# Optimization experiments

Hardware: AMD Instinct MI355X
Metric: run time of the kernel (lower is better)

The kernel has to match this reference:

```python
import jax, jax.numpy as jnp
import numpy as np

# dims
N = 50000      # total nodes in merged batch graph
M = 250000     # edges for GNN propagation
E = 200000     # candidate edges scored by mixture-Bernoulli head
MAXN = 512     # max_num_nodes (padded adjacency row length)
H = 128        # hidden_dim = embedding_dim = msg_dim
EF = 128       # edge_feat_dim = 2 * att_edge_dim
ATT = 128      # att_hidden_dim
K = 20         # num_mix_component
L = 3          # num_GNN_layers
S = 512        # num_subgraph
B = 16         # batch of graphs
C = 1          # num_canonical_order


def setup_inputs() -> dict:
    key = jax.random.key(0)
    ks = list(jax.random.split(key, 64))
    it = iter(ks)
    nk = lambda: next(it)
    d = {}
    d['node_feat'] = jax.random.normal(nk(), (N, MAXN), jnp.float32)
    d['edge'] = jax.random.randint(nk(), (M, 2), 0, N, dtype=jnp.int32)
    d['edge_feat'] = jax.random.normal(nk(), (M, EF), jnp.float32)
    d['node_idx_gnn'] = jax.random.randint(nk(), (E, 2), 0, N, dtype=jnp.int32)
    d['label'] = (jax.random.uniform(nk(), (E,)) < 0.1).astype(jnp.float32)
    # even sorted partition of E candidate edges into S subgraphs (all nonempty)
    d['subgraph_idx'] = ((jnp.arange(E) * S) // E).astype(jnp.int32)
    # bc_idx = repeat_interleave(arange(B*C), subgraphs_per_graph)
    d['bc_idx'] = jnp.repeat(jnp.arange(B * C, dtype=jnp.int32), S // (B * C))
    # params
    def lin(k, out_d, in_d):
        return jax.random.normal(k, (out_d, in_d), jnp.float32) * (1.0 / np.sqrt(in_d))
    d['dec_W'] = lin(nk(), H, MAXN); d['dec_b'] = jnp.zeros((H,), jnp.float32)
    d['msg_W1'] = jnp.stack([lin(nk(), H, H + EF) for _ in range(L)])
    d['msg_b1'] = jnp.zeros((L, H), jnp.float32)
    d['msg_W2'] = jnp.stack([lin(nk(), H, H) for _ in range(L)])
    d['msg_b2'] = jnp.zeros((L, H), jnp.float32)
    d['att_W1'] = jnp.stack([lin(nk(), ATT, H + EF) for _ in range(L)])
    d['att_b1'] = jnp.zeros((L, ATT), jnp.float32)
    d['att_W2'] = jnp.stack([lin(nk(), H, ATT) for _ in range(L)])
    d['att_b2'] = jnp.zeros((L, H), jnp.float32)
    d['gru_Wih'] = jnp.stack([lin(nk(), 3 * H, H) for _ in range(L)])
    d['gru_bih'] = jnp.zeros((L, 3 * H), jnp.float32)
    d['gru_Whh'] = jnp.stack([lin(nk(), 3 * H, H) for _ in range(L)])
    d['gru_bhh'] = jnp.zeros((L, 3 * H), jnp.float32)
    d['th_W1'] = lin(nk(), H, H); d['th_b1'] = jnp.zeros((H,), jnp.float32)
    d['th_W2'] = lin(nk(), H, H); d['th_b2'] = jnp.zeros((H,), jnp.float32)
    d['th_W3'] = lin(nk(), K, H); d['th_b3'] = jnp.zeros((K,), jnp.float32)
    d['al_W1'] = lin(nk(), H, H); d['al_b1'] = jnp.zeros((H,), jnp.float32)
    d['al_W2'] = lin(nk(), H, H); d['al_b2'] = jnp.zeros((H,), jnp.float32)
    d['al_W3'] = lin(nk(), K, H); d['al_b3'] = jnp.zeros((K,), jnp.float32)
    return d


def _gran_forward(node_feat, edge_feat, label, dec_W, dec_b, msg_W1, msg_b1,
                  msg_W2, msg_b2, att_W1, att_b1, att_W2, att_b2, gru_Wih,
                  gru_bih, gru_Whh, gru_bhh, th_W1, th_b1, th_W2, th_b2,
                  th_W3, th_b3, al_W1, al_b1, al_W2, al_b2, al_W3, al_b3,
                  edge, node_idx_gnn, subgraph_idx, bc_idx):
    n = node_feat.shape[0]
    # decoder_input: Linear(max_num_nodes -> embedding_dim)
    state = node_feat @ dec_W.T + dec_b  # [N, H]
    src, dst = edge[:, 0], edge[:, 1]
    for l in range(L):
        if l > 0:
            state = jax.nn.relu(state)
        # _prop: gather diff, msg MLP, sigmoid attention gate, scatter-sum, GRU
        diff = state[src] - state[dst]                       # [M, H]
        ei = jnp.concatenate([diff, edge_feat], axis=1)      # [M, H+EF]
        msg = jax.nn.relu(ei @ msg_W1[l].T + msg_b1[l]) @ msg_W2[l].T + msg_b2[l]
        att = jax.nn.sigmoid(jax.nn.relu(ei @ att_W1[l].T + att_b1[l]) @ att_W2[l].T + att_b2[l])
        agg = jax.ops.segment_sum(msg * att, dst, num_segments=n)  # [N, H]
        # torch GRUCell
        gi = agg @ gru_Wih[l].T + gru_bih[l]
        gh = state @ gru_Whh[l].T + gru_bhh[l]
        i_r, i_z, i_n = jnp.split(gi, 3, axis=-1)
        h_r, h_z, h_n = jnp.split(gh, 3, axis=-1)
        r = jax.nn.sigmoid(i_r + h_r)
        z = jax.nn.sigmoid(i_z + h_z)
        nn_ = jnp.tanh(i_n + r * h_n)
        state = (1.0 - z) * nn_ + z * state
    # mixture-Bernoulli heads on candidate-edge node-state diffs
    d2 = state[node_idx_gnn[:, 0]] - state[node_idx_gnn[:, 1]]  # [E, H]
    def mlp3(x, W1, b1, W2, b2, W3, b3):
        h = jax.nn.relu(x @ W1.T + b1)
        h = jax.nn.relu(h @ W2.T + b2)
        return h @ W3.T + b3
    log_theta = mlp3(d2, th_W1, th_b1, th_W2, th_b2, th_W3, th_b3)  # [E, K]
    log_alpha = mlp3(d2, al_W1, al_b1, al_W2, al_b2, al_W3, al_b3)  # [E, K]
    # mixture_bernoulli_loss (pos_weight = 1.0)
    y = label[:, None]
    adj_loss = jax.nn.softplus(-log_theta) + (1.0 - y) * log_theta  # BCEWithLogits, [E, K]
    const = jax.ops.segment_sum(jnp.ones((label.shape[0],), log_theta.dtype), subgraph_idx, num_segments=S)
    reduce_adj = jax.ops.segment_sum(adj_loss, subgraph_idx, num_segments=S)     # [S, K]
    reduce_la = jax.ops.segment_sum(log_alpha, subgraph_idx, num_segments=S)
    reduce_la = jax.nn.log_softmax(reduce_la / const[:, None], axis=-1)
    log_prob = jax.scipy.special.logsumexp(-reduce_adj + reduce_la, axis=1)      # [S]
    bc_log_prob = jax.ops.segment_sum(log_prob, bc_idx, num_segments=B * C)
    bc_const = jax.ops.segment_sum(const, bc_idx, num_segments=B * C)
    bc_loss = (bc_log_prob / bc_const).reshape(B, C)
    b_loss = jax.scipy.special.logsumexp(bc_loss, axis=1)  # logsumexp over orderings
    return jnp.mean(-b_loss)


def reference(node_feat, edge, edge_feat, node_idx_gnn, label, subgraph_idx,
              bc_idx, dec_W, dec_b, msg_W1, msg_b1, msg_W2, msg_b2, att_W1,
              att_b1, att_W2, att_b2, gru_Wih, gru_bih, gru_Whh, gru_bhh,
              th_W1, th_b1, th_W2, th_b2, th_W3, th_b3, al_W1, al_b1, al_W2,
              al_b2, al_W3, al_b3):
    return _gran_forward(node_feat, edge_feat, label, dec_W, dec_b, msg_W1,
                         msg_b1, msg_W2, msg_b2, att_W1, att_b1, att_W2,
                         att_b2, gru_Wih, gru_bih, gru_Whh, gru_bhh, th_W1,
                         th_b1, th_W2, th_b2, th_W3, th_b3, al_W1, al_b1,
                         al_W2, al_b2, al_W3, al_b3, edge, node_idx_gnn,
                         subgraph_idx, bc_idx)
```

## Files before the change

### kernel.cpp

```cpp
#include <hip/hip_runtime.h>
#include <cstdint>
#include <cstddef>


typedef __bf16 bf16x8 __attribute__((ext_vector_type(8)));
typedef short  s16x8  __attribute__((ext_vector_type(8)));
typedef short  s16x4  __attribute__((ext_vector_type(4)));
typedef float  f32x4  __attribute__((ext_vector_type(4)));

__device__ inline unsigned short f2bf(float f) {
    return __builtin_bit_cast(unsigned short, (__bf16)f);
}
__device__ inline float bf2f(unsigned short b) {
    return __uint_as_float(((unsigned int)b) << 16);
}
__device__ inline unsigned int pk2(float a, float b) {
    return ((unsigned int)f2bf(b) << 16) | f2bf(a);
}
__device__ inline f32x4 MFMA(bf16x8 a, bf16x8 b, f32x4 c) {
    return __builtin_amdgcn_mfma_f32_16x16x32_bf16(a, b, c, 0, 0, 0);
}

__device__ inline bf16x8 ld_swz(const char* lds, int row, int unit) {
    return *(const bf16x8*)(lds + row * 256 + ((unit ^ (row & 7)) << 4));
}
__device__ inline void hid_write(char* HID, int h0, int erow, s16x4 s4) {
    int unit = h0 >> 3;
    *(s16x4*)(HID + erow * 256 + ((unit ^ (erow & 7)) << 4) + ((h0 & 4) << 1)) = s4;
}
__device__ inline bf16x8 ldA(const short* __restrict__ Wb, int K, int row, int koff) {
    return *(const bf16x8*)(Wb + (size_t)row * K + koff);
}
__device__ inline bf16x8 ld_f32_frag(const float* __restrict__ p) {
    float4 a = *(const float4*)p, b = *(const float4*)(p + 4);
    s16x8 s;
    s[0] = f2bf(a.x); s[1] = f2bf(a.y); s[2] = f2bf(a.z); s[3] = f2bf(a.w);
    s[4] = f2bf(b.x); s[5] = f2bf(b.y); s[6] = f2bf(b.z); s[7] = f2bf(b.w);
    return __builtin_bit_cast(bf16x8, s);
}

#define NPACK 31
struct PrepackArgs {
    const float* src[NPACK];
    short*       dst[NPACK];
    int stride[NPACK];
    int rows[NPACK];
    int rowsTot[NPACK];
    int cols[NPACK];
};

__global__ void prepack(PrepackArgs a) {
    int e = blockIdx.y;
    int row = blockIdx.x;
    if (row >= a.rowsTot[e]) return;
    int c8 = threadIdx.x;
    if (c8 * 8 >= a.cols[e]) return;
    s16x8 s = {};
    if (row < a.rows[e]) {
        const float* p = a.src[e] + (size_t)row * a.stride[e] + c8 * 8;
        float4 x = *(const float4*)p, y = *(const float4*)(p + 4);
        s[0] = f2bf(x.x); s[1] = f2bf(x.y); s[2] = f2bf(x.z); s[3] = f2bf(x.w);
        s[4] = f2bf(y.x); s[5] = f2bf(y.y); s[6] = f2bf(y.z); s[7] = f2bf(y.w);
    }
    *(s16x8*)(a.dst[e] + (size_t)row * a.cols[e] + c8 * 8) = s;
}

__device__ inline void proj_gemm_store(const char* ST, char* PJ,
                                       const short* __restrict__ projW,
                                       short* __restrict__ proj,
                                       int rb, int R, int tid)
{
    const int l = tid & 63, w = tid >> 6;
    f32x4 accP[2][2][4] = {};
#pragma unroll
    for (int ks = 0; ks < 4; ++ks) {
        int koff = ks * 32 + (l >> 4) * 8;
        bf16x8 aw[2][2];
#pragma unroll
        for (int pc = 0; pc < 2; ++pc)
#pragma unroll
            for (int mt = 0; mt < 2; ++mt)
                aw[pc][mt] = ldA(projW, 128, pc * 128 + 32 * w + 16 * mt + (l & 15), koff);
#pragma unroll
        for (int n = 0; n < 4; ++n) {
            bf16x8 b = ld_swz(ST, 16 * n + (l & 15), ks * 4 + (l >> 4));
#pragma unroll
            for (int pc = 0; pc < 2; ++pc)
#pragma unroll
                for (int mt = 0; mt < 2; ++mt)
                    accP[pc][mt][n] = MFMA(aw[pc][mt], b, accP[pc][mt][n]);
        }
    }
    const int half = w >> 1;
#pragma unroll
    for (int hh = 0; hh < 2; ++hh) {
        __syncthreads();
        if (half == hh) {
#pragma unroll
            for (int pc = 0; pc < 2; ++pc)
#pragma unroll
                for (int mt = 0; mt < 2; ++mt) {
                    int h0 = 32 * w + 16 * mt + ((l >> 4) << 2);
                    int colp = 2 * h0 + 4 * pc - 128 * hh;
#pragma unroll
                    for (int n = 0; n < 4; ++n) {
                        f32x4 v = accP[pc][mt][n];
                        s16x4 s4;
                        s4[0] = f2bf(v[0]); s4[1] = f2bf(v[1]);
                        s4[2] = f2bf(v[2]); s4[3] = f2bf(v[3]);
                        hid_write(PJ, colp, 16 * n + (l & 15), s4);
                    }
                }
        }
        __syncthreads();
#pragma unroll
        for (int p2 = 0; p2 < 4; ++p2) {
            int row = p2 * 16 + (tid >> 4);
            int r = rb + row;
            if (r < R) {
                bf16x8 v = ld_swz(PJ, row, tid & 15);
                *(s16x8*)(proj + (size_t)r * 256 + hh * 128 + (tid & 15) * 8) =
                    __builtin_bit_cast(s16x8, v);
            }
        }
    }
}

__global__ __launch_bounds__(256, 2)
void dec_proj(const float* __restrict__ nf, int R,
              const short* __restrict__ decWb, const float* __restrict__ bias,
              const short* __restrict__ projW,
              short* __restrict__ sOut, short* __restrict__ proj)
{
    __shared__ char ST[16384];
    __shared__ char PJ[16384];
    const int tid = threadIdx.x, l = tid & 63, w = tid >> 6;
    const int rb = blockIdx.x * 64;

    const float* brow[4];
#pragma unroll
    for (int n = 0; n < 4; ++n) {
        int row = rb + 16 * n + (l & 15); if (row >= R) row = R - 1;
        brow[n] = nf + (size_t)row * 512;
    }

    f32x4 acc[2][4] = {};
    for (int kc = 0; kc < 512; kc += 128) {
#pragma unroll
        for (int ks = 0; ks < 4; ++ks) {
            int koff = kc + ks * 32 + (l >> 4) * 8;
            bf16x8 a0 = ldA(decWb, 512, 32 * w + (l & 15), koff);
            bf16x8 a1 = ldA(decWb, 512, 32 * w + 16 + (l & 15), koff);
#pragma unroll
            for (int n = 0; n < 4; ++n) {
                bf16x8 b = ld_f32_frag(brow[n] + koff);
                acc[0][n] = MFMA(a0, b, acc[0][n]);
                acc[1][n] = MFMA(a1, b, acc[1][n]);
            }
        }
    }
#pragma unroll
    for (int mt = 0; mt < 2; ++mt) {
        int c0 = 32 * w + 16 * mt + ((l >> 4) << 2);
        float4 bv = *(const float4*)&bias[c0];
#pragma unroll
        for (int n = 0; n < 4; ++n) {
            f32x4 v = acc[mt][n];
            s16x4 s4;
            s4[0] = f2bf(v[0] + bv.x); s4[1] = f2bf(v[1] + bv.y);
            s4[2] = f2bf(v[2] + bv.z); s4[3] = f2bf(v[3] + bv.w);
            hid_write(ST, c0, 16 * n + (l & 15), s4);
        }
    }
    __syncthreads();
#pragma unroll
    for (int p2 = 0; p2 < 4; ++p2) {
        int row = p2 * 16 + (tid >> 4);
        int r = rb + row;
        if (r < R) {
            bf16x8 v = ld_swz(ST, row, tid & 15);
            *(s16x8*)(sOut + (size_t)r * 128 + (tid & 15) * 8) =
                __builtin_bit_cast(s16x8, v);
        }
    }
    proj_gemm_store(ST, PJ, projW, proj, rb, R, tid);
}

template<int HAS_PROJ>
__global__ __launch_bounds__(256, 2)
void node_fused(const short* __restrict__ aggb, const short* __restrict__ sin_,
                const short* __restrict__ Wih, const short* __restrict__ Whh,
                const float* __restrict__ bih, const float* __restrict__ bhh,
                const short* __restrict__ projW,
                short* __restrict__ sOut, short* __restrict__ proj, int R)
{
    __shared__ char ST[16384];
    __shared__ char PJ[16384];
    const int tid = threadIdx.x, l = tid & 63, w = tid >> 6;
    const int rb = blockIdx.x * 64;

    const short* arow[4];
    const short* srow[4];
#pragma unroll
    for (int n = 0; n < 4; ++n) {
        int row = rb + 16 * n + (l & 15); if (row >= R) row = R - 1;
        arow[n] = aggb + (size_t)row * 128;
        srow[n] = sin_ + (size_t)row * 128;
    }
    s16x4 svv[2][4];
#pragma unroll
    for (int mt = 0; mt < 2; ++mt) {
        int c0 = 32 * w + 16 * mt + ((l >> 4) << 2);
#pragma unroll
        for (int n = 0; n < 4; ++n)
            svv[mt][n] = *(const s16x4*)(srow[n] + c0);
    }

    unsigned int rpk[2][4][2], zpk[2][4][2];

    for (int p = 0; p < 3; ++p) {
        f32x4 gia[2][4] = {}, gha[2][4] = {};
#pragma unroll
        for (int ks = 0; ks < 4; ++ks) {
            int koff = ks * 32 + (l >> 4) * 8;
            bf16x8 ai0 = ldA(Wih, 128, p * 128 + 32 * w + (l & 15), koff);
            bf16x8 ai1 = ldA(Wih, 128, p * 128 + 32 * w + 16 + (l & 15), koff);
            bf16x8 ah0 = ldA(Whh, 128, p * 128 + 32 * w + (l & 15), koff);
            bf16x8 ah1 = ldA(Whh, 128, p * 128 + 32 * w + 16 + (l & 15), koff);
#pragma unroll
            for (int n = 0; n < 4; ++n) {
                bf16x8 ba = *(const bf16x8*)(arow[n] + koff);
                bf16x8 bs = *(const bf16x8*)(srow[n] + koff);
                gia[0][n] = MFMA(ai0, ba, gia[0][n]);
                gia[1][n] = MFMA(ai1, ba, gia[1][n]);
                gha[0][n] = MFMA(ah0, bs, gha[0][n]);
                gha[1][n] = MFMA(ah1, bs, gha[1][n]);
            }
        }
#pragma unroll
        for (int mt = 0; mt < 2; ++mt) {
            int c0 = 32 * w + 16 * mt + ((l >> 4) << 2);
            float4 bi = *(const float4*)&bih[p * 128 + c0];
            float4 bh = *(const float4*)&bhh[p * 128 + c0];
            float biv[4] = {bi.x, bi.y, bi.z, bi.w};
            float bhv[4] = {bh.x, bh.y, bh.z, bh.w};
#pragma unroll
            for (int n = 0; n < 4; ++n) {
                float gv[4], hv[4];
#pragma unroll
                for (int q = 0; q < 4; ++q) {
                    gv[q] = gia[mt][n][q] + biv[q];
                    hv[q] = gha[mt][n][q] + bhv[q];
                }
                if (p == 0) {
                    rpk[mt][n][0] = pk2(1.f / (1.f + expf(-(gv[0] + hv[0]))),
                                        1.f / (1.f + expf(-(gv[1] + hv[1]))));
                    rpk[mt][n][1] = pk2(1.f / (1.f + expf(-(gv[2] + hv[2]))),
                                        1.f / (1.f + expf(-(gv[3] + hv[3]))));
                } else if (p == 1) {
                    zpk[mt][n][0] = pk2(1.f / (1.f + expf(-(gv[0] + hv[0]))),
                                        1.f / (1.f + expf(-(gv[1] + hv[1]))));
                    zpk[mt][n][1] = pk2(1.f / (1.f + expf(-(gv[2] + hv[2]))),
                                        1.f / (1.f + expf(-(gv[3] + hv[3]))));
                } else {
                    s16x4 s4;
#pragma unroll
                    for (int q = 0; q < 4; ++q) {
                        unsigned int ru = rpk[mt][n][q >> 1], zu = zpk[mt][n][q >> 1];
                        float r = bf2f((unsigned short)((q & 1) ? (ru >> 16) : (ru & 0xffffu)));
                        float z = bf2f((unsigned short)((q & 1) ? (zu >> 16) : (zu & 0xffffu)));
                        float nn = tanhf(gv[q] + r * hv[q]);
                        float o = (1.f - z) * nn + z * bf2f((unsigned short)svv[mt][n][q]);
                        s4[q] = f2bf(HAS_PROJ ? fmaxf(o, 0.f) : o);
                    }
                    hid_write(ST, c0, 16 * n + (l & 15), s4);
                }
            }
        }
    }
    __syncthreads();
#pragma unroll
    for (int p2 = 0; p2 < 4; ++p2) {
        int row = p2 * 16 + (tid >> 4);
        int r = rb + row;
        if (r < R) {
            bf16x8 v = ld_swz(ST, row, tid & 15);
            *(s16x8*)(sOut + (size_t)r * 128 + (tid & 15) * 8) =
                __builtin_bit_cast(s16x8, v);
        }
    }
    if (HAS_PROJ)
        proj_gemm_store(ST, PJ, projW, proj, rb, R, tid);
}

__global__ __launch_bounds__(256, 3)
void edge_fused2(const short* __restrict__ efc,
                 const int* __restrict__ srcs, const int* __restrict__ dsts,
                 const short* __restrict__ proj,
                 const short* __restrict__ mW1b, const short* __restrict__ mW2,
                 const short* __restrict__ aW1b, const short* __restrict__ aW2,
                 const float* __restrict__ mb1, const float* __restrict__ mb2,
                 const float* __restrict__ ab1, const float* __restrict__ ab2,
                 short* __restrict__ msgatt, int M, int ntiles)
{
    __shared__ char HIDm[16384];
    __shared__ char HIDa[16384];
    const int tid = threadIdx.x, l = tid & 63, w = tid >> 6;
    int q = ntiles >> 3, r = ntiles & 7;
    int xcd = blockIdx.x & 7, o = blockIdx.x >> 3;
    int tile = (xcd < r ? xcd * (q + 1) : r * (q + 1) + (xcd - r) * q) + o;
    const int pb = tile * 64;

    const char* erow[4];
    s16x8 psv[2][4], pdv[2][4];
    {
#pragma unroll
        for (int n = 0; n < 4; ++n) {
            int pos = pb + 16 * n + (l & 15); if (pos >= M) pos = M - 1;
            int sv = srcs[pos], dv = dsts[pos];
            erow[n] = (const char*)(efc + (size_t)pos * 128);
#pragma unroll
            for (int mt = 0; mt < 2; ++mt) {
                int off = 2 * (32 * w + 16 * mt + ((l >> 4) << 2));
                psv[mt][n] = *(const s16x8*)(proj + (size_t)sv * 256 + off);
                pdv[mt][n] = *(const s16x8*)(proj + (size_t)dv * 256 + off);
            }
        }
    }

    f32x4 accm[2][4] = {}, acca[2][4] = {};
#pragma unroll
    for (int ks = 0; ks < 4; ++ks) {
        int koff = ks * 32 + (l >> 4) * 8;
        bf16x8 am0 = ldA(mW1b, 128, 32 * w + (l & 15), koff);
        bf16x8 am1 = ldA(mW1b, 128, 32 * w + 16 + (l & 15), koff);
        bf16x8 aa0 = ldA(aW1b, 128, 32 * w + (l & 15), koff);
        bf16x8 aa1 = ldA(aW1b, 128, 32 * w + 16 + (l & 15), koff);
#pragma unroll
        for (int n = 0; n < 4; ++n) {
            bf16x8 b = *(const bf16x8*)(erow[n] + koff * 2);
            accm[0][n] = MFMA(am0, b, accm[0][n]);
            accm[1][n] = MFMA(am1, b, accm[1][n]);
            acca[0][n] = MFMA(aa0, b, acca[0][n]);
            acca[1][n] = MFMA(aa1, b, acca[1][n]);
        }
    }
#pragma unroll
    for (int mt = 0; mt < 2; ++mt) {
        int h0 = 32 * w + 16 * mt + ((l >> 4) << 2);
        float4 bm = *(const float4*)&mb1[h0];
        float4 ba = *(const float4*)&ab1[h0];
        float bmv[4] = {bm.x, bm.y, bm.z, bm.w};
        float bav[4] = {ba.x, ba.y, ba.z, ba.w};
#pragma unroll
        for (int n = 0; n < 4; ++n) {
            s16x8 ps = psv[mt][n], pd = pdv[mt][n];
            f32x4 vm = accm[mt][n], va = acca[mt][n];
            s16x4 sm, sa;
#pragma unroll
            for (int qq = 0; qq < 4; ++qq) {
                float m_ = vm[qq] + bmv[qq] + bf2f((unsigned short)ps[qq])
                           - bf2f((unsigned short)pd[qq]);
                float a_ = va[qq] + bav[qq] + bf2f((unsigned short)ps[qq + 4])
                           - bf2f((unsigned short)pd[qq + 4]);
                sm[qq] = f2bf(fmaxf(m_, 0.f));
                sa[qq] = f2bf(fmaxf(a_, 0.f));
            }
            hid_write(HIDm, h0, 16 * n + (l & 15), sm);
            hid_write(HIDa, h0, 16 * n + (l & 15), sa);
        }
    }
    __syncthreads();

    f32x4 acc2m[2][4] = {}, acc2a[2][4] = {};
#pragma unroll
    for (int ks = 0; ks < 4; ++ks) {
        int koff = ks * 32 + (l >> 4) * 8;
        bf16x8 wm0 = ldA(mW2, 128, 32 * w + (l & 15), koff);
        bf16x8 wm1 = ldA(mW2, 128, 32 * w + 16 + (l & 15), koff);
        bf16x8 wa0 = ldA(aW2, 128, 32 * w + (l & 15), koff);
        bf16x8 wa1 = ldA(aW2, 128, 32 * w + 16 + (l & 15), koff);
#pragma unroll
        for (int n = 0; n < 4; ++n) {
            bf16x8 bm = ld_swz(HIDm, 16 * n + (l & 15), ks * 4 + (l >> 4));
            bf16x8 ba = ld_swz(HIDa, 16 * n + (l & 15), ks * 4 + (l >> 4));
            acc2m[0][n] = MFMA(wm0, bm, acc2m[0][n]);
            acc2m[1][n] = MFMA(wm1, bm, acc2m[1][n]);
            acc2a[0][n] = MFMA(wa0, ba, acc2a[0][n]);
            acc2a[1][n] = MFMA(wa1, ba, acc2a[1][n]);
        }
    }
    __syncthreads();
#pragma unroll
    for (int mt = 0; mt < 2; ++mt) {
        int c0 = 32 * w + 16 * mt + ((l >> 4) << 2);
        float4 bm2 = *(const float4*)&mb2[c0];
        float4 ba2 = *(const float4*)&ab2[c0];
#pragma unroll
        for (int n = 0; n < 4; ++n) {
            f32x4 m_ = acc2m[mt][n], a_ = acc2a[mt][n];
            float o0 = (m_[0] + bm2.x) / (1.f + expf(-(a_[0] + ba2.x)));
            float o1 = (m_[1] + bm2.y) / (1.f + expf(-(a_[1] + ba2.y)));
            float o2 = (m_[2] + bm2.z) / (1.f + expf(-(a_[2] + ba2.z)));
            float o3 = (m_[3] + bm2.w) / (1.f + expf(-(a_[3] + ba2.w)));
            s16x4 s4;
            s4[0] = f2bf(o0); s4[1] = f2bf(o1); s4[2] = f2bf(o2); s4[3] = f2bf(o3);
            hid_write(HIDm, c0, 16 * n + (l & 15), s4);
        }
    }
    __syncthreads();
#pragma unroll
    for (int p2 = 0; p2 < 4; ++p2) {
        int row = p2 * 16 + (tid >> 4);
        int pos = pb + row;
        if (pos < M) {
            bf16x8 v = ld_swz(HIDm, row, tid & 15);
            *(s16x8*)(msgatt + (size_t)pos * 128 + (tid & 15) * 8) =
                __builtin_bit_cast(s16x8, v);
        }
    }
}

__global__ __launch_bounds__(256, 4)
void mlp_loss(const short* __restrict__ sP, const int* __restrict__ gidx,
              const float* __restrict__ label, const int* __restrict__ sg,
              const short* __restrict__ thW1, const short* __restrict__ thW2,
              const short* __restrict__ thW3,
              const float* __restrict__ thb1, const float* __restrict__ thb2,
              const float* __restrict__ thb3,
              const short* __restrict__ alW1, const short* __restrict__ alW2,
              const short* __restrict__ alW3,
              const float* __restrict__ alb1, const float* __restrict__ alb2,
              const float* __restrict__ alb3,
              float* __restrict__ radj, float* __restrict__ rla,
              float* __restrict__ cntS, int E, int S)
{
    __shared__ char D2T[16384];
    __shared__ char HID[16384];
    __shared__ float sadj[2][20];
    __shared__ float sla[2][20];
    __shared__ float scnt[2];
    __shared__ int sbase;
    const int tid = threadIdx.x, l = tid & 63, w = tid >> 6;
    const int eb = blockIdx.x * 64;

    if (tid == 0) sbase = sg[eb];
    if (tid < 40) { sadj[tid / 20][tid % 20] = 0.f; sla[tid / 20][tid % 20] = 0.f; }
    if (tid < 2) scnt[tid] = 0.f;

    for (int i = tid; i < 64 * 16; i += 256) {
        int row = i >> 4, u = i & 15;
        int e = eb + row; if (e >= E) e = E - 1;
        int2 ab = *(const int2*)&gidx[2 * (size_t)e];
        s16x8 x = *(const s16x8*)(sP + (size_t)ab.x * 128 + u * 8);
        s16x8 y = *(const s16x8*)(sP + (size_t)ab.y * 128 + u * 8);
        s16x8 d;
#pragma unroll
        for (int j = 0; j < 8; ++j)
            d[j] = f2bf(bf2f((unsigned short)x[j]) - bf2f((unsigned short)y[j]));
        *(s16x8*)(D2T + row * 256 + ((u ^ (row & 7)) << 4)) = d;
    }
    __syncthreads();

    for (int pass = 0; pass < 2; ++pass) {
        const short* W1 = pass ? alW1 : thW1;
        const short* W2 = pass ? alW2 : thW2;
        const short* W3 = pass ? alW3 : thW3;
        const float* b1 = pass ? alb1 : thb1;
        const float* b2 = pass ? alb2 : thb2;
        const float* b3 = pass ? alb3 : thb3;

        f32x4 acc[2][4] = {};
#pragma unroll
        for (int ks = 0; ks < 4; ++ks) {
            int koff = ks * 32 + (l >> 4) * 8;
            bf16x8 a0 = ldA(W1, 128, 32 * w + (l & 15), koff);
            bf16x8 a1 = ldA(W1, 128, 32 * w + 16 + (l & 15), koff);
#pragma unroll
            for (int n = 0; n < 4; ++n) {
                bf16x8 b = ld_swz(D2T, 16 * n + (l & 15), ks * 4 + (l >> 4));
                acc[0][n] = MFMA(a0, b, acc[0][n]);
                acc[1][n] = MFMA(a1, b, acc[1][n]);
            }
        }
        __syncthreads();
#pragma unroll
        for (int mt = 0; mt < 2; ++mt) {
            int h0 = 32 * w + 16 * mt + ((l >> 4) << 2);
            float4 bv = *(const float4*)&b1[h0];
#pragma unroll
            for (int n = 0; n < 4; ++n) {
                f32x4 v = acc[mt][n];
                s16x4 s4;
                s4[0] = f2bf(fmaxf(v[0] + bv.x, 0.f));
                s4[1] = f2bf(fmaxf(v[1] + bv.y, 0.f));
                s4[2] = f2bf(fmaxf(v[2] + bv.z, 0.f));
                s4[3] = f2bf(fmaxf(v[3] + bv.w, 0.f));
                hid_write(HID, h0, 16 * n + (l & 15), s4);
            }
        }
        __syncthreads();
        f32x4 acc2[2][4] = {};
#pragma unroll
        for (int ks = 0; ks < 4; ++ks) {
            int koff = ks * 32 + (l >> 4) * 8;
            bf16x8 a0 = ldA(W2, 128, 32 * w + (l & 15), koff);
            bf16x8 a1 = ldA(W2, 128, 32 * w + 16 + (l & 15), koff);
#pragma unroll
            for (int n = 0; n < 4; ++n) {
                bf16x8 b = ld_swz(HID, 16 * n + (l & 15), ks * 4 + (l >> 4));
                acc2[0][n] = MFMA(a0, b, acc2[0][n]);
                acc2[1][n] = MFMA(a1, b, acc2[1][n]);
            }
        }
        __syncthreads();
#pragma unroll
        for (int mt = 0; mt < 2; ++mt) {
            int h0 = 32 * w + 16 * mt + ((l >> 4) << 2);
            float4 bv = *(const float4*)&b2[h0];
#pragma unroll
            for (int n = 0; n < 4; ++n) {
                f32x4 v = acc2[mt][n];
                s16x4 s4;
                s4[0] = f2bf(fmaxf(v[0] + bv.x, 0.f));
                s4[1] = f2bf(fmaxf(v[1] + bv.y, 0.f));
                s4[2] = f2bf(fmaxf(v[2] + bv.z, 0.f));
                s4[3] = f2bf(fmaxf(v[3] + bv.w, 0.f));
                hid_write(HID, h0, 16 * n + (l & 15), s4);
            }
        }
        __syncthreads();
        f32x4 acc3[2] = {};
#pragma unroll
        for (int ks = 0; ks < 4; ++ks) {
            int koff = ks * 32 + (l >> 4) * 8;
            bf16x8 a0 = ldA(W3, 128, (l & 15), koff);
            bf16x8 a1 = ldA(W3, 128, 16 + (l & 15), koff);
            bf16x8 b = ld_swz(HID, 16 * w + (l & 15), ks * 4 + (l >> 4));
            acc3[0] = MFMA(a0, b, acc3[0]);
            acc3[1] = MFMA(a1, b, acc3[1]);
        }
        {
            int e = eb + 16 * w + (l & 15);
            if (e < E) {
                int ls = sg[e] - sbase;
                if (ls < 0) ls = 0; if (ls > 1) ls = 1;
                float y = (pass == 0) ? label[e] : 0.f;
#pragma unroll
                for (int mt = 0; mt < 2; ++mt) {
                    int c0 = 16 * mt + ((l >> 4) << 2);
                    if (c0 < 20) {
#pragma unroll
                        for (int qq = 0; qq < 4; ++qq) {
                            int k = c0 + qq;
                            if (k < 20) {
                                float t = acc3[mt][qq] + b3[k];
                                if (pass == 0) {
                                    float sp = fmaxf(-t, 0.f) + log1pf(expf(-fabsf(t)));
                                    atomicAdd(&sadj[ls][k], sp + (1.f - y) * t);
                                } else {
                                    atomicAdd(&sla[ls][k], t);
                                }
                            }
                        }
                    }
                }
            }
        }
        __syncthreads();
    }

    if (tid < 64) {
        int e = eb + tid;
        if (e < E) {
            int ls = sg[e] - sbase;
            if (ls >= 0 && ls < 2) atomicAdd(&scnt[ls], 1.f);
        }
    }
    __syncthreads();
    if (tid < 40) {
        int ls = tid / 20, k = tid % 20;
        int s = sbase + ls;
        if (s < S) {
            float v = sadj[ls][k], v2 = sla[ls][k];
            if (v  != 0.f) atomicAdd(&radj[s * 20 + k], v);
            if (v2 != 0.f) atomicAdd(&rla[s * 20 + k], v2);
        }
    }
    if (tid < 2) {
        int s = sbase + tid;
        if (s < S && scnt[tid] != 0.f) atomicAdd(&cntS[s], scnt[tid]);
    }
}

__global__ void csr_count(const int* __restrict__ edge, int* __restrict__ cnt, int M) {
    int e = blockIdx.x * 256 + threadIdx.x;
    if (e < M) atomicAdd(&cnt[edge[2 * (size_t)e + 1]], 1);
}

__global__ void csr_scan(const int* __restrict__ cnt, int* __restrict__ rowptr,
                         int* __restrict__ wofs, int N)
{
    __shared__ int part[1024];
    int t = threadIdx.x;
    int chunk = (N + 1023) / 1024;
    int b0 = t * chunk, b1 = b0 + chunk; if (b1 > N) b1 = N; if (b0 > N) b0 = N;
    int s = 0;
    for (int i = b0; i < b1; ++i) s += cnt[i];
    part[t] = s;
    __syncthreads();
    for (int off = 1; off < 1024; off <<= 1) {
        int v = (t >= off) ? part[t - off] : 0;
        __syncthreads();
        part[t] += v;
        __syncthreads();
    }
    int run = (t ? part[t - 1] : 0);
    for (int i = b0; i < b1; ++i) { rowptr[i] = run; wofs[i] = run; run += cnt[i]; }
    if (t == 1023) rowptr[N] = run;
}

__global__ void csr_scatter2(const int* __restrict__ edge, int* __restrict__ wofs,
                             int* __restrict__ eidx, int* __restrict__ srcs,
                             int* __restrict__ dsts, int M)
{
    int e = blockIdx.x * 256 + threadIdx.x;
    if (e < M) {
        int2 sd = *(const int2*)&edge[2 * (size_t)e];
        int p = atomicAdd(&wofs[sd.y], 1);
        eidx[p] = e; srcs[p] = sd.x; dsts[p] = sd.y;
    }
}

__global__ void ef_gather(const float* __restrict__ ef, const int* __restrict__ eidx,
                          short* __restrict__ efc, int M)
{
    long i = (long)blockIdx.x * 256 + threadIdx.x;
    if (i >= (long)M * 16) return;
    int p = (int)(i >> 4), u = (int)(i & 15);
    int e = eidx[p];
    const float* sp = ef + (size_t)e * 128 + u * 8;
    float4 a = *(const float4*)sp, b = *(const float4*)(sp + 4);
    s16x8 s;
    s[0] = f2bf(a.x); s[1] = f2bf(a.y); s[2] = f2bf(a.z); s[3] = f2bf(a.w);
    s[4] = f2bf(b.x); s[5] = f2bf(b.y); s[6] = f2bf(b.z); s[7] = f2bf(b.w);
    *(s16x8*)(efc + (size_t)p * 128 + u * 8) = s;
}

__global__ __launch_bounds__(256)
void agg_gather3(const short* __restrict__ msgatt, const int* __restrict__ rowptr,
                 short* __restrict__ aggb, int N)
{
    int wid = blockIdx.x * 4 + (threadIdx.x >> 6);
    int l = threadIdx.x & 63;
    int v = wid * 4 + (l >> 4);
    int u = l & 15;
    if (v >= N) return;
    int b = rowptr[v], e = rowptr[v + 1];
    float acc[8] = {};
    for (int i = b; i < e; ++i) {
        s16x8 x = *(const s16x8*)(msgatt + (size_t)i * 128 + u * 8);
#pragma unroll
        for (int j = 0; j < 8; ++j) acc[j] += bf2f((unsigned short)x[j]);
    }
    s16x8 o;
#pragma unroll
    for (int j = 0; j < 8; ++j) o[j] = f2bf(acc[j]);
    *(s16x8*)(aggb + (size_t)v * 128 + u * 8) = o;
}

__global__ void final_kernel(const float* __restrict__ radj, const float* __restrict__ rla,
                             const float* __restrict__ cnt, const int* __restrict__ bc_idx,
                             float* __restrict__ out)
{
    __shared__ float bcl[16], bcc[16];
    const int s = threadIdx.x;
    if (s < 16) { bcl[s] = 0.f; bcc[s] = 0.f; }
    __syncthreads();
    float c = cnt[s];
    float x[20];
    float mx = -1e30f;
#pragma unroll
    for (int k = 0; k < 20; ++k) { x[k] = rla[s * 20 + k] / c; mx = fmaxf(mx, x[k]); }
    float se = 0.f;
#pragma unroll
    for (int k = 0; k < 20; ++k) se += expf(x[k] - mx);
    float lse = mx + logf(se);
    float t[20];
    float m2 = -1e30f;
#pragma unroll
    for (int k = 0; k < 20; ++k) { t[k] = -radj[s * 20 + k] + x[k] - lse; m2 = fmaxf(m2, t[k]); }
    float s2 = 0.f;
#pragma unroll
    for (int k = 0; k < 20; ++k) s2 += expf(t[k] - m2);
    float lp = m2 + logf(s2);
    atomicAdd(&bcl[bc_idx[s]], lp);
    atomicAdd(&bcc[bc_idx[s]], c);
    __syncthreads();
    if (s == 0) {
        float a = 0.f;
        for (int b = 0; b < 16; ++b) a += bcl[b] / bcc[b];
        out[0] = -a / 16.f;
    }
}

extern "C" void kernel_launch(void* const* d_in, const int* in_sizes, int n_in,
                              void* d_out, int out_size, void* d_ws, size_t ws_size,
                              hipStream_t stream)
{
    const float* node_feat = (const float*)d_in[0];
    const int*   edge      = (const int*)  d_in[1];
    const float* edge_feat = (const float*)d_in[2];
    const int*   gnn_idx   = (const int*)  d_in[3];
    const float* label     = (const float*)d_in[4];
    const int*   sg_idx    = (const int*)  d_in[5];
    const int*   bc_idx    = (const int*)  d_in[6];
    const float* dec_W  = (const float*)d_in[7];
    const float* dec_b  = (const float*)d_in[8];
    const float* msg_W1 = (const float*)d_in[9];
    const float* msg_b1 = (const float*)d_in[10];
    const float* msg_W2 = (const float*)d_in[11];
    const float* msg_b2 = (const float*)d_in[12];
    const float* att_W1 = (const float*)d_in[13];
    const float* att_b1 = (const float*)d_in[14];
    const float* att_W2 = (const float*)d_in[15];
    const float* att_b2 = (const float*)d_in[16];
    const float* gru_Wih = (const float*)d_in[17];
    const float* gru_bih = (const float*)d_in[18];
    const float* gru_Whh = (const float*)d_in[19];
    const float* gru_bhh = (const float*)d_in[20];
    const float* th_W1 = (const float*)d_in[21];
    const float* th_b1 = (const float*)d_in[22];
    const float* th_W2 = (const float*)d_in[23];
    const float* th_b2 = (const float*)d_in[24];
    const float* th_W3 = (const float*)d_in[25];
    const float* th_b3 = (const float*)d_in[26];
    const float* al_W1 = (const float*)d_in[27];
    const float* al_b1 = (const float*)d_in[28];
    const float* al_W2 = (const float*)d_in[29];
    const float* al_b2 = (const float*)d_in[30];
    const float* al_W3 = (const float*)d_in[31];
    const float* al_b3 = (const float*)d_in[32];

    const int N = in_sizes[0] / 512;
    const int M = in_sizes[1] / 2;
    const int E = in_sizes[3] / 2;
    const int S = in_sizes[6];

    size_t off = 0;
    auto alloc = [&](size_t bytes) {
        char* p = (char*)d_ws + off;
        off += (bytes + 255) & ~(size_t)255;
        return p;
    };
    short* decWb  = (short*)alloc((size_t)128 * 512 * 2);
    short* projWb = (short*)alloc((size_t)3 * 256 * 128 * 2);
    short* mW1bB  = (short*)alloc((size_t)3 * 128 * 128 * 2);
    short* aW1bB  = (short*)alloc((size_t)3 * 128 * 128 * 2);
    short* mW2B   = (short*)alloc((size_t)3 * 128 * 128 * 2);
    short* aW2B   = (short*)alloc((size_t)3 * 128 * 128 * 2);
    short* gihB   = (short*)alloc((size_t)3 * 384 * 128 * 2);
    short* ghhB   = (short*)alloc((size_t)3 * 384 * 128 * 2);
    short* thW1B  = (short*)alloc((size_t)128 * 128 * 2);
    short* thW2B  = (short*)alloc((size_t)128 * 128 * 2);
    short* thW3B  = (short*)alloc((size_t)32 * 128 * 2);
    short* alW1B  = (short*)alloc((size_t)128 * 128 * 2);
    short* alW2B  = (short*)alloc((size_t)128 * 128 * 2);
    short* alW3B  = (short*)alloc((size_t)32 * 128 * 2);
    short* sA     = (short*)alloc((size_t)N * 128 * 2);
    short* sB     = (short*)alloc((size_t)N * 128 * 2);
    short* sP     = (short*)alloc((size_t)N * 128 * 2);
    short* efc    = (short*)alloc((size_t)M * 128 * 2);
    short* msgatt = (short*)alloc((size_t)M * 128 * 2);
    short* proj   = (short*)alloc((size_t)N * 256 * 2);
    short* aggb   = (short*)alloc((size_t)N * 128 * 2);
    int*   cntN   = (int*)  alloc((size_t)N * 4);
    int*   wofs   = (int*)  alloc((size_t)N * 4);
    int*   rowptr = (int*)  alloc((size_t)(N + 1) * 4);
    int*   eidx   = (int*)  alloc((size_t)M * 4);
    int*   srcs   = (int*)  alloc((size_t)M * 4);
    int*   dsts   = (int*)  alloc((size_t)M * 4);
    float* radj   = (float*)alloc((size_t)S * 20 * 4);
    float* rla    = (float*)alloc((size_t)S * 20 * 4);
    float* cntS   = (float*)alloc((size_t)S * 4);

    PrepackArgs pa;
    int ei = 0;
    auto add = [&](const float* s, short* d, int stride, int rows, int rowsTot, int cols) {
        pa.src[ei] = s; pa.dst[ei] = d; pa.stride[ei] = stride;
        pa.rows[ei] = rows; pa.rowsTot[ei] = rowsTot; pa.cols[ei] = cols; ++ei;
    };
    add(dec_W, decWb, 512, 128, 128, 512);
    for (int l = 0; l < 3; ++l) {
        add(msg_W1 + (size_t)l * 128 * 256,       projWb + (size_t)l * 256 * 128,          256, 128, 128, 128);
        add(att_W1 + (size_t)l * 128 * 256,       projWb + (size_t)l * 256 * 128 + 16384,  256, 128, 128, 128);
        add(msg_W1 + (size_t)l * 128 * 256 + 128, mW1bB + (size_t)l * 16384,               256, 128, 128, 128);
        add(att_W1 + (size_t)l * 128 * 256 + 128, aW1bB + (size_t)l * 16384,               256, 128, 128, 128);
        add(msg_W2 + (size_t)l * 16384,           mW2B + (size_t)l * 16384,                128, 128, 128, 128);
        add(att_W2 + (size_t)l * 16384,           aW2B + (size_t)l * 16384,                128, 128, 128, 128);
        add(gru_Wih + (size_t)l * 49152,          gihB + (size_t)l * 49152,                128, 384, 384, 128);
        add(gru_Whh + (size_t)l * 49152,          ghhB + (size_t)l * 49152,                128, 384, 384, 128);
    }
    add(th_W1, thW1B, 128, 128, 128, 128);
    add(th_W2, thW2B, 128, 128, 128, 128);
    add(th_W3, thW3B, 128, 20, 32, 128);
    add(al_W1, alW1B, 128, 128, 128, 128);
    add(al_W2, alW2B, 128, 128, 128, 128);
    add(al_W3, alW3B, 128, 20, 32, 128);

    const dim3 blk(256);
    const int gN64 = (N + 63) / 64;
    const int gE64 = (E + 63) / 64;
    const int gMt  = (M + 255) / 256;
    const int ntilesM = (M + 63) / 64;
    const int gAgg = (N + 15) / 16;

    hipMemsetAsync(radj, 0, (size_t)(S * 20 * 2 + S) * 4, stream);
    hipMemsetAsync(cntN, 0, (size_t)N * 4, stream);

    prepack<<<dim3(384, NPACK), dim3(64), 0, stream>>>(pa);

    csr_count   <<<gMt, blk, 0, stream>>>(edge, cntN, M);
    csr_scan    <<<1, 1024, 0, stream>>>(cntN, rowptr, wofs, N);
    csr_scatter2<<<gMt, blk, 0, stream>>>(edge, wofs, eidx, srcs, dsts, M);
    ef_gather   <<<(int)(((long)M * 16 + 255) / 256), blk, 0, stream>>>(edge_feat, eidx, efc, M);

    dec_proj<<<gN64, blk, 0, stream>>>(node_feat, N, decWb, dec_b, projWb, sA, proj);

    short* bufs[2] = { sA, sB };
    for (int l = 0; l < 3; ++l) {
        short* sin  = bufs[l & 1];
        short* sout = (l == 2) ? sP : bufs[(l + 1) & 1];
        edge_fused2<<<ntilesM, blk, 0, stream>>>(efc, srcs, dsts, proj,
            mW1bB + (size_t)l * 16384, mW2B + (size_t)l * 16384,
            aW1bB + (size_t)l * 16384, aW2B + (size_t)l * 16384,
            msg_b1 + l * 128, msg_b2 + l * 128,
            att_b1 + l * 128, att_b2 + l * 128,
            msgatt, M, ntilesM);
        agg_gather3<<<gAgg, blk, 0, stream>>>(msgatt, rowptr, aggb, N);
        if (l < 2) {
            node_fused<1><<<gN64, blk, 0, stream>>>(aggb, sin,
                gihB + (size_t)l * 49152, ghhB + (size_t)l * 49152,
                gru_bih + l * 384, gru_bhh + l * 384,
                projWb + (size_t)(l + 1) * 256 * 128, sout, proj, N);
        } else {
            node_fused<0><<<gN64, blk, 0, stream>>>(aggb, sin,
                gihB + (size_t)l * 49152, ghhB + (size_t)l * 49152,
                gru_bih + l * 384, gru_bhh + l * 384,
                nullptr, sout, nullptr, N);
        }
    }

    mlp_loss<<<gE64, blk, 0, stream>>>(sP, gnn_idx, label, sg_idx,
        thW1B, thW2B, thW3B, th_b1, th_b2, th_b3,
        alW1B, alW2B, alW3B, al_b1, al_b2, al_b3,
        radj, rla, cntS, E, S);
    final_kernel<<<1, S, 0, stream>>>(radj, rla, cntS, bc_idx, (float*)d_out);
}
```

Before: 1.205 ms.

## Raise dec_proj occupancy, defer dst proj loads, shuffle-reduce mixture loss

```diff
diff --git a/kernel.cpp b/kernel.cpp
--- a/kernel.cpp
+++ b/kernel.cpp
@@ -126,7 +126,7 @@
     }
 }
 
-__global__ __launch_bounds__(256, 2)
+__global__ __launch_bounds__(256, 3)
 void dec_proj(const float* __restrict__ nf, int R,
               const short* __restrict__ decWb, const float* __restrict__ bias,
               const short* __restrict__ projW,
@@ -312,18 +312,19 @@
     const int pb = tile * 64;
 
     const char* erow[4];
-    s16x8 psv[2][4], pdv[2][4];
+    int dstv[4];
+    s16x8 psv[2][4];
     {
 #pragma unroll
         for (int n = 0; n < 4; ++n) {
             int pos = pb + 16 * n + (l & 15); if (pos >= M) pos = M - 1;
-            int sv = srcs[pos], dv = dsts[pos];
+            int sv = srcs[pos];
+            dstv[n] = dsts[pos];
             erow[n] = (const char*)(efc + (size_t)pos * 128);
 #pragma unroll
             for (int mt = 0; mt < 2; ++mt) {
                 int off = 2 * (32 * w + 16 * mt + ((l >> 4) << 2));
                 psv[mt][n] = *(const s16x8*)(proj + (size_t)sv * 256 + off);
-                pdv[mt][n] = *(const s16x8*)(proj + (size_t)dv * 256 + off);
             }
         }
     }
@@ -354,7 +355,8 @@
         float bav[4] = {ba.x, ba.y, ba.z, ba.w};
 #pragma unroll
         for (int n = 0; n < 4; ++n) {
-            s16x8 ps = psv[mt][n], pd = pdv[mt][n];
+            s16x8 ps = psv[mt][n];
+            s16x8 pd = *(const s16x8*)(proj + (size_t)dstv[n] * 256 + 2 * h0);
             f32x4 vm = accm[mt][n], va = acca[mt][n];
             s16x4 sm, sa;
 #pragma unroll
@@ -437,16 +439,23 @@
 {
     __shared__ char D2T[16384];
     __shared__ char HID[16384];
-    __shared__ float sadj[2][20];
-    __shared__ float sla[2][20];
+    __shared__ float sacc[2][2][20];
     __shared__ float scnt[2];
     __shared__ int sbase;
     const int tid = threadIdx.x, l = tid & 63, w = tid >> 6;
     const int eb = blockIdx.x * 64;
 
     if (tid == 0) sbase = sg[eb];
-    if (tid < 40) { sadj[tid / 20][tid % 20] = 0.f; sla[tid / 20][tid % 20] = 0.f; }
-    if (tid < 2) scnt[tid] = 0.f;
+    if (tid < 80) sacc[tid / 40][(tid / 20) & 1][tid % 20] = 0.f;
+
+    if (w == 0) {
+        int e = eb + l;
+        bool valid = e < E;
+        int lsv = valid ? sg[e] - sg[eb] : -1;
+        unsigned long long m0 = __ballot(lsv == 0);
+        unsigned long long m1 = __ballot(lsv == 1);
+        if (l == 0) { scnt[0] = (float)__popcll(m0); scnt[1] = (float)__popcll(m1); }
+    }
 
     for (int i = tid; i < 64 * 16; i += 256) {
         int row = i >> 4, u = i & 15;
@@ -542,39 +551,37 @@
         }
         {
             int e = eb + 16 * w + (l & 15);
-            if (e < E) {
-                int ls = sg[e] - sbase;
-                if (ls < 0) ls = 0; if (ls > 1) ls = 1;
-                float y = (pass == 0) ? label[e] : 0.f;
-#pragma unroll
-                for (int mt = 0; mt < 2; ++mt) {
-                    int c0 = 16 * mt + ((l >> 4) << 2);
-                    if (c0 < 20) {
-#pragma unroll
-                        for (int qq = 0; qq < 4; ++qq) {
-                            int k = c0 + qq;
-                            if (k < 20) {
-                                float t = acc3[mt][qq] + b3[k];
-                                if (pass == 0) {
-                                    float sp = fmaxf(-t, 0.f) + log1pf(expf(-fabsf(t)));
-                                    atomicAdd(&sadj[ls][k], sp + (1.f - y) * t);
-                                } else {
-                                    atomicAdd(&sla[ls][k], t);
-                                }
-                            }
+            bool val = e < E;
+            float lsf = val ? (float)(sg[e] - sbase) : 0.f;
+            float yv = (pass == 0 && val) ? label[e] : 0.f;
+#pragma unroll
+            for (int mt = 0; mt < 2; ++mt) {
+#pragma unroll
+                for (int qq = 0; qq < 4; ++qq) {
+                    int k = 16 * mt + ((l >> 4) << 2) + qq;
+                    bool kok = k < 20;
+                    float bk = kok ? b3[k] : 0.f;
+                    float vv = 0.f;
+                    if (val && kok) {
+                        float t = acc3[mt][qq] + bk;
+                        if (pass == 0) {
+                            float sp = fmaxf(-t, 0.f) + log1pf(expf(-fabsf(t)));
+                            vv = sp + (1.f - yv) * t;
+                        } else {
+                            vv = t;
                         }
                     }
+                    float vA = vv * (1.f - lsf), vB = vv * lsf;
+                    vA += __shfl_xor(vA, 1); vB += __shfl_xor(vB, 1);
+                    vA += __shfl_xor(vA, 2); vB += __shfl_xor(vB, 2);
+                    vA += __shfl_xor(vA, 4); vB += __shfl_xor(vB, 4);
+                    vA += __shfl_xor(vA, 8); vB += __shfl_xor(vB, 8);
+                    if ((l & 15) == 0 && kok) {
+                        atomicAdd(&sacc[pass][0][k], vA);
+                        if (vB != 0.f) atomicAdd(&sacc[pass][1][k], vB);
+                    }
                 }
             }
-        }
-        __syncthreads();
-    }
-
-    if (tid < 64) {
-        int e = eb + tid;
-        if (e < E) {
-            int ls = sg[e] - sbase;
-            if (ls >= 0 && ls < 2) atomicAdd(&scnt[ls], 1.f);
         }
     }
     __syncthreads();
@@ -582,7 +589,8 @@
         int ls = tid / 20, k = tid % 20;
         int s = sbase + ls;
         if (s < S) {
-            float v = sadj[ls][k], v2 = sla[ls][k];
+            float v  = sacc[0][ls][k];
+            float v2 = sacc[1][ls][k];
             if (v  != 0.f) atomicAdd(&radj[s * 20 + k], v);
             if (v2 != 0.f) atomicAdd(&rla[s * 20 + k], v2);
         }
```

Result: no change. 1.220 ms (+1.3%).
